# Kernel optimization log

Measured on AMD Instinct MI355X. Metric: run time of the kernel, lower is better.

## Reference

```python
import jax, jax.numpy as jnp
import numpy as np

DK = 64

def setup_inputs() -> dict:
    key = jax.random.key(0)
    kq, kk, kv = jax.random.split(key, 3)
    B, S, dk, dv = 16, 2048, 64, 64
    q = jax.random.normal(kq, (B, S, dk), dtype=jnp.float32)
    k = jax.random.normal(kk, (B, S, dk), dtype=jnp.float32)
    v = jax.random.normal(kv, (B, S, dv), dtype=jnp.float32)
    return {"q": q, "k": k, "v": v}

def reference(q, k, v):
    # scores: [B, Sq, Sk], scaled by 1/sqrt(dk)
    scale = 1.0 / jnp.sqrt(jnp.asarray(DK, dtype=q.dtype))
    scores = jnp.einsum('bqd,bkd->bqk', q, k) * scale
    attn = jax.nn.softmax(scores, axis=-1)
    return jnp.einsum('bqk,bkd->bqd', attn, v)
```

## Files before the change

kernel.cpp:

```cpp
#include <hip/hip_runtime.h>
#include <hip/hip_fp16.h>

#define SLEN 2048

typedef _Float16 half8_t  __attribute__((ext_vector_type(8)));
typedef __fp16   fp16x2_t __attribute__((ext_vector_type(2)));
typedef float    floatx16 __attribute__((ext_vector_type(16)));
typedef float    float2v  __attribute__((ext_vector_type(2)));

#define MFMA(a, b, c) __builtin_amdgcn_mfma_f32_32x32x16_f16((a), (b), (c), 0, 0, 0)

typedef const __attribute__((address_space(1))) void gvoid_t;
typedef __attribute__((address_space(3))) void lvoid_t;

__device__ __forceinline__ void gload_lds16(const void* g, void* l) {
    __builtin_amdgcn_global_load_lds((gvoid_t*)g, (lvoid_t*)l, 16, 0, 0);
}

__device__ __forceinline__ int bswap23(int r) {
    return (r & ~12) | ((r & 4) << 1) | ((r & 8) >> 1);
}

#define QSCALE 0.18033688011112042f
#define CINIT  -5.770780163555854f

__device__ __forceinline__ floatx16 zero16() {
    floatx16 z;
    #pragma unroll
    for (int i = 0; i < 16; ++i) z[i] = 0.0f;
    return z;
}

__device__ __forceinline__ floatx16 initC() {
    floatx16 z;
    #pragma unroll
    for (int i = 0; i < 16; ++i) z[i] = CINIT;
    return z;
}

union PU { fp16x2_t h2[4]; half8_t h8; };

__global__ __launch_bounds__(256)
void prep_kernel(const float* __restrict__ Kg, const float* __restrict__ Vg,
                 _Float16* __restrict__ KP, _Float16* __restrict__ VP)
{
    __shared__ _Float16 kt[32][72];
    __shared__ _Float16 vt[32][72];
    const int t = threadIdx.x;
    const int T = blockIdx.x;
    const size_t row0 = (size_t)T * 32;

    {
        const int r = t >> 3, c0 = (t & 7) * 8;
        const float* kp = Kg + (row0 + r) * 64 + c0;
        const float* vp = Vg + (row0 + r) * 64 + c0;
        float4 a0 = *(const float4*)kp;
        float4 a1 = *(const float4*)(kp + 4);
        float4 b0 = *(const float4*)vp;
        float4 b1 = *(const float4*)(vp + 4);
        kt[r][c0 + 0] = (_Float16)a0.x; kt[r][c0 + 1] = (_Float16)a0.y;
        kt[r][c0 + 2] = (_Float16)a0.z; kt[r][c0 + 3] = (_Float16)a0.w;
        kt[r][c0 + 4] = (_Float16)a1.x; kt[r][c0 + 5] = (_Float16)a1.y;
        kt[r][c0 + 6] = (_Float16)a1.z; kt[r][c0 + 7] = (_Float16)a1.w;
        vt[r][c0 + 0] = (_Float16)b0.x; vt[r][c0 + 1] = (_Float16)b0.y;
        vt[r][c0 + 2] = (_Float16)b0.z; vt[r][c0 + 3] = (_Float16)b0.w;
        vt[r][c0 + 4] = (_Float16)b1.x; vt[r][c0 + 5] = (_Float16)b1.y;
        vt[r][c0 + 6] = (_Float16)b1.z; vt[r][c0 + 7] = (_Float16)b1.w;
    }
    __syncthreads();

    const int hi  = (t >> 5) & 1;
    const int col = t & 31;

    {
        const int dc = t >> 6;
        half8_t ko;
        #pragma unroll
        for (int j = 0; j < 8; ++j) ko[j] = kt[col][dc * 16 + hi * 8 + j];
        *(half8_t*)(KP + (size_t)T * 2048 + t * 8) = ko;
    }
    {
        const int g = t >> 6, kc = g & 1, nc = g >> 1;
        half8_t vo;
        #pragma unroll
        for (int j = 0; j < 8; ++j)
            vo[j] = vt[bswap23(kc * 16 + hi * 8 + j)][nc * 32 + col];
        *(half8_t*)(VP + (size_t)T * 2048 + t * 8) = vo;
    }
}

__global__ __launch_bounds__(256, 2)
void fattn_kernel(const float* __restrict__ Qg, const _Float16* __restrict__ KP,
                  const _Float16* __restrict__ VP, float* __restrict__ Og)
{
    __shared__ __align__(16) _Float16 ring[4 * 2 * 4096];
    __shared__ float lbufl[4][2][32];
    __shared__ float lbuf2[2][32];

    const int tid  = threadIdx.x;
    const int w    = tid >> 6;
    const int lane = tid & 63;
    const int h    = lane >> 5;
    const int col  = lane & 31;

    const int p  = blockIdx.x;
    const int b  = ((p >> 8) << 3) | (p & 7);
    const int qb = (p >> 3) & 31;

    half8_t qh[2][4];
    #pragma unroll
    for (int s = 0; s < 2; ++s) {
        const size_t qrow = (size_t)b * SLEN + (size_t)qb * 64 + s * 32 + col;
        const float* qp = Qg + qrow * 64 + h * 8;
        #pragma unroll
        for (int dc = 0; dc < 4; ++dc) {
            float4 f0 = *(const float4*)(qp + dc * 16);
            float4 f1 = *(const float4*)(qp + dc * 16 + 4);
            float v[8] = {f0.x, f0.y, f0.z, f0.w, f1.x, f1.y, f1.z, f1.w};
            #pragma unroll
            for (int j = 0; j < 8; ++j)
                qh[s][dc][j] = (_Float16)(v[j] * QSCALE);
        }
    }

    _Float16* myring = ring + w * 8192;
    const char* KPb = (const char*)KP;
    const char* VPb = (const char*)VP;

    auto stage = [&](int buf, int t) {
        const size_t off = ((size_t)(b * 64 + w * 16 + t)) << 12;
        const char* ks = KPb + off + lane * 16;
        const char* vs = VPb + off + lane * 16;
        _Float16* d = myring + buf * 4096;
        gload_lds16(ks,        d);
        gload_lds16(ks + 1024, d + 512);
        gload_lds16(ks + 2048, d + 1024);
        gload_lds16(ks + 3072, d + 1536);
        gload_lds16(vs,        d + 2048);
        gload_lds16(vs + 1024, d + 2560);
        gload_lds16(vs + 2048, d + 3072);
        gload_lds16(vs + 3072, d + 3584);
    };

    floatx16 o00 = zero16(), o01 = zero16(), o10 = zero16(), o11 = zero16();
    float2v la0A = {0.0f, 0.0f}, la0B = {0.0f, 0.0f};
    float2v la1A = {0.0f, 0.0f}, la1B = {0.0f, 0.0f};

    stage(0, 0);

#define EXPPK(SS, U, J, ACC) {                                        \
    float e0 = __builtin_amdgcn_exp2f(SS[2*(J)]);                     \
    float e1 = __builtin_amdgcn_exp2f(SS[2*(J)+1]);                   \
    float2v e2 = {e0, e1};                                            \
    ACC += e2;                                                        \
    (U).h2[(J) & 3] = __builtin_amdgcn_cvt_pkrtz(e0, e1); }

    for (int t = 0; t < 16; ++t) {
        const int cur = t & 1;
        if (t < 15) {
            stage(1 - cur, t + 1);
            asm volatile("s_waitcnt vmcnt(8)" ::: "memory");
        } else {
            asm volatile("s_waitcnt vmcnt(0)" ::: "memory");
        }

        _Float16* kb = myring + cur * 4096;
        _Float16* vb = kb + 2048;

        half8_t kf[4];
        #pragma unroll
        for (int dc = 0; dc < 4; ++dc)
            kf[dc] = *(half8_t*)(kb + dc * 512 + lane * 8);

        floatx16 sa0 = zero16(), sb0 = initC();
        floatx16 sa1 = zero16(), sb1 = initC();

        sa0 = MFMA(kf[0], qh[0][0], sa0);
        sb0 = MFMA(kf[2], qh[0][2], sb0);
        sa0 = MFMA(kf[1], qh[0][1], sa0);
        sb0 = MFMA(kf[3], qh[0][3], sb0);

        half8_t vf[4];
        #pragma unroll
        for (int g = 0; g < 4; ++g)
            vf[g] = *(half8_t*)(vb + g * 512 + lane * 8);

        floatx16 ss0 = sa0 + sb0;
        PU u0, u1;
        sa1 = MFMA(kf[0], qh[1][0], sa1);
        EXPPK(ss0, u0, 0, la0A) EXPPK(ss0, u0, 1, la0B)
        sb1 = MFMA(kf[2], qh[1][2], sb1);
        EXPPK(ss0, u0, 2, la0A) EXPPK(ss0, u0, 3, la0B)
        sa1 = MFMA(kf[1], qh[1][1], sa1);
        EXPPK(ss0, u1, 4, la0A) EXPPK(ss0, u1, 5, la0B)
        sb1 = MFMA(kf[3], qh[1][3], sb1);
        EXPPK(ss0, u1, 6, la0A) EXPPK(ss0, u1, 7, la0B)

        half8_t pf00 = u0.h8, pf01 = u1.h8;

        floatx16 ss1 = sa1 + sb1;
        PU u2, u3;
        o00 = MFMA(pf00, vf[0], o00);
        EXPPK(ss1, u2, 0, la1A) EXPPK(ss1, u2, 1, la1B)
        o01 = MFMA(pf00, vf[2], o01);
        EXPPK(ss1, u2, 2, la1A) EXPPK(ss1, u2, 3, la1B)
        o00 = MFMA(pf01, vf[1], o00);
        EXPPK(ss1, u3, 4, la1A) EXPPK(ss1, u3, 5, la1B)
        o01 = MFMA(pf01, vf[3], o01);
        EXPPK(ss1, u3, 6, la1A) EXPPK(ss1, u3, 7, la1B)

        half8_t pf10 = u2.h8, pf11 = u3.h8;

        o10 = MFMA(pf10, vf[0], o10);
        o11 = MFMA(pf10, vf[2], o11);
        o10 = MFMA(pf11, vf[1], o10);
        o11 = MFMA(pf11, vf[3], o11);
    }
#undef EXPPK

    float la0 = la0A[0] + la0A[1] + la0B[0] + la0B[1];
    float la1 = la1A[0] + la1A[1] + la1B[0] + la1B[1];

    float lw0 = la0 + __shfl_xor(la0, 32, 64);
    float lw1 = la1 + __shfl_xor(la1, 32, 64);

    float* cb = (float*)ring;

#define ODUMP(d, g, acc) { _Pragma("unroll") \
    for (int r = 0; r < 16; ++r) (d)[(((g)*16 + r)*2 + h)*32 + col] = (acc)[r]; }
#define OADD(d, g, acc) { _Pragma("unroll") \
    for (int r = 0; r < 16; ++r) (acc)[r] += (d)[(((g)*16 + r)*2 + h)*32 + col]; }

    __syncthreads();
    if (w >= 2) {
        float* d = cb + (w - 2) * 4096;
        ODUMP(d, 0, o00) ODUMP(d, 1, o01) ODUMP(d, 2, o10) ODUMP(d, 3, o11)
        if (h == 0) { lbufl[w][0][col] = lw0; lbufl[w][1][col] = lw1; }
    }
    __syncthreads();
    if (w < 2) {
        float* d = cb + w * 4096;
        OADD(d, 0, o00) OADD(d, 1, o01) OADD(d, 2, o10) OADD(d, 3, o11)
        lw0 += lbufl[w + 2][0][col];
        lw1 += lbufl[w + 2][1][col];
    }
    __syncthreads();
    if (w == 1) {
        ODUMP(cb, 0, o00) ODUMP(cb, 1, o01) ODUMP(cb, 2, o10) ODUMP(cb, 3, o11)
        if (h == 0) { lbufl[1][0][col] = lw0; lbufl[1][1][col] = lw1; }
    }
    __syncthreads();
    if (w == 0) {
        OADD(cb, 0, o00) OADD(cb, 1, o01) OADD(cb, 2, o10) OADD(cb, 3, o11)
        lw0 += lbufl[1][0][col];
        lw1 += lbufl[1][1][col];
        if (h == 0) { lbuf2[0][col] = lw0; lbuf2[1][col] = lw1; }
    }
    __syncthreads();
    if (w == 0) {
        float* ob = cb + 8192;
        #pragma unroll
        for (int r = 0; r < 16; ++r) {
            const int qr = (r & 3) + 8 * (r >> 2) + 4 * h;
            const float li0 = 1.0f / lbuf2[0][qr];
            const float li1 = 1.0f / lbuf2[1][qr];
            ob[(0 * 32 + qr) * 64 +  0 + col] = o00[r] * li0;
            ob[(0 * 32 + qr) * 64 + 32 + col] = o01[r] * li0;
            ob[(1 * 32 + qr) * 64 +  0 + col] = o10[r] * li1;
            ob[(1 * 32 + qr) * 64 + 32 + col] = o11[r] * li1;
        }
    }
    __syncthreads();
    {
        const float* ob = cb + 8192;
        const int q = tid >> 2, ch = tid & 3;
        float4 x0 = *(const float4*)(ob + q * 64 + ch * 16);
        float4 x1 = *(const float4*)(ob + q * 64 + ch * 16 + 4);
        float4 x2 = *(const float4*)(ob + q * 64 + ch * 16 + 8);
        float4 x3 = *(const float4*)(ob + q * 64 + ch * 16 + 12);
        float* op = Og + ((size_t)b * SLEN + (size_t)qb * 64 + q) * 64 + ch * 16;
        *(float4*)(op)      = x0;
        *(float4*)(op + 4)  = x1;
        *(float4*)(op + 8)  = x2;
        *(float4*)(op + 12) = x3;
    }
#undef ODUMP
#undef OADD
}

extern "C" void kernel_launch(void* const* d_in, const int* in_sizes, int n_in,
                              void* d_out, int out_size, void* d_ws, size_t ws_size,
                              hipStream_t stream) {
    const float* q = (const float*)d_in[0];
    const float* k = (const float*)d_in[1];
    const float* v = (const float*)d_in[2];
    float* o = (float*)d_out;

    _Float16* KP = (_Float16*)d_ws;
    _Float16* VP = KP + (size_t)1024 * 2048;
    (void)ws_size; (void)in_sizes; (void)n_in; (void)out_size;

    prep_kernel<<<dim3(1024), dim3(256), 0, stream>>>(k, v, KP, VP);
    fattn_kernel<<<dim3(512), dim3(256), 0, stream>>>(q, KP, VP, o);
}
```

Baseline: 103.9 us.

## Merge two query tiles per 512-thread block and split K/V wait counts

```diff
diff --git a/kernel.cpp b/kernel.cpp
--- a/kernel.cpp
+++ b/kernel.cpp
@@ -89,28 +89,30 @@
     }
 }
 
-__global__ __launch_bounds__(256, 2)
+__global__ __launch_bounds__(512, 2)
 void fattn_kernel(const float* __restrict__ Qg, const _Float16* __restrict__ KP,
                   const _Float16* __restrict__ VP, float* __restrict__ Og)
 {
-    __shared__ __align__(16) _Float16 ring[4 * 2 * 4096];
-    __shared__ float lbufl[4][2][32];
-    __shared__ float lbuf2[2][32];
+    __shared__ __align__(16) _Float16 ring[8 * 8192];
+    __shared__ float lbufl[2][4][2][32];
+    __shared__ float lbuf2[2][2][32];
 
     const int tid  = threadIdx.x;
     const int w    = tid >> 6;
     const int lane = tid & 63;
     const int h    = lane >> 5;
     const int col  = lane & 31;
+    const int quarter = w & 3;
+    const int qh      = w >> 2;
 
     const int p  = blockIdx.x;
-    const int b  = ((p >> 8) << 3) | (p & 7);
-    const int qb = (p >> 3) & 31;
-
-    half8_t qh[2][4];
+    const int b  = (p & 7) | ((p >> 7) << 3);
+    const int qb = (p >> 3) & 15;
+
+    half8_t qh_[2][4];
     #pragma unroll
     for (int s = 0; s < 2; ++s) {
-        const size_t qrow = (size_t)b * SLEN + (size_t)qb * 64 + s * 32 + col;
+        const size_t qrow = (size_t)b * SLEN + (size_t)qb * 128 + qh * 64 + s * 32 + col;
         const float* qp = Qg + qrow * 64 + h * 8;
         #pragma unroll
         for (int dc = 0; dc < 4; ++dc) {
@@ -119,7 +121,7 @@
             float v[8] = {f0.x, f0.y, f0.z, f0.w, f1.x, f1.y, f1.z, f1.w};
             #pragma unroll
             for (int j = 0; j < 8; ++j)
-                qh[s][dc][j] = (_Float16)(v[j] * QSCALE);
+                qh_[s][dc][j] = (_Float16)(v[j] * QSCALE);
         }
     }
 
@@ -128,7 +130,7 @@
     const char* VPb = (const char*)VP;
 
     auto stage = [&](int buf, int t) {
-        const size_t off = ((size_t)(b * 64 + w * 16 + t)) << 12;
+        const size_t off = ((size_t)(b * 64 + quarter * 16 + t)) << 12;
         const char* ks = KPb + off + lane * 16;
         const char* vs = VPb + off + lane * 16;
         _Float16* d = myring + buf * 4096;
@@ -146,6 +148,8 @@
     float2v la0A = {0.0f, 0.0f}, la0B = {0.0f, 0.0f};
     float2v la1A = {0.0f, 0.0f}, la1B = {0.0f, 0.0f};
 
+    if (qh) __builtin_amdgcn_s_sleep(15);
+
     stage(0, 0);
 
 #define EXPPK(SS, U, J, ACC) {                                        \
@@ -159,9 +163,9 @@
         const int cur = t & 1;
         if (t < 15) {
             stage(1 - cur, t + 1);
-            asm volatile("s_waitcnt vmcnt(8)" ::: "memory");
+            asm volatile("s_waitcnt vmcnt(12)" ::: "memory");
         } else {
-            asm volatile("s_waitcnt vmcnt(0)" ::: "memory");
+            asm volatile("s_waitcnt vmcnt(4)" ::: "memory");
         }
 
         _Float16* kb = myring + cur * 4096;
@@ -175,11 +179,13 @@
         floatx16 sa0 = zero16(), sb0 = initC();
         floatx16 sa1 = zero16(), sb1 = initC();
 
-        sa0 = MFMA(kf[0], qh[0][0], sa0);
-        sb0 = MFMA(kf[2], qh[0][2], sb0);
-        sa0 = MFMA(kf[1], qh[0][1], sa0);
-        sb0 = MFMA(kf[3], qh[0][3], sb0);
-
+        sa0 = MFMA(kf[0], qh_[0][0], sa0);
+        sb0 = MFMA(kf[2], qh_[0][2], sb0);
+        sa0 = MFMA(kf[1], qh_[0][1], sa0);
+        sb0 = MFMA(kf[3], qh_[0][3], sb0);
+
+        if (t < 15) asm volatile("s_waitcnt vmcnt(8)" ::: "memory");
+        else        asm volatile("s_waitcnt vmcnt(0)" ::: "memory");
         half8_t vf[4];
         #pragma unroll
         for (int g = 0; g < 4; ++g)
@@ -187,13 +193,13 @@
 
         floatx16 ss0 = sa0 + sb0;
         PU u0, u1;
-        sa1 = MFMA(kf[0], qh[1][0], sa1);
+        sa1 = MFMA(kf[0], qh_[1][0], sa1);
         EXPPK(ss0, u0, 0, la0A) EXPPK(ss0, u0, 1, la0B)
-        sb1 = MFMA(kf[2], qh[1][2], sb1);
+        sb1 = MFMA(kf[2], qh_[1][2], sb1);
         EXPPK(ss0, u0, 2, la0A) EXPPK(ss0, u0, 3, la0B)
-        sa1 = MFMA(kf[1], qh[1][1], sa1);
+        sa1 = MFMA(kf[1], qh_[1][1], sa1);
         EXPPK(ss0, u1, 4, la0A) EXPPK(ss0, u1, 5, la0B)
-        sb1 = MFMA(kf[3], qh[1][3], sb1);
+        sb1 = MFMA(kf[3], qh_[1][3], sb1);
         EXPPK(ss0, u1, 6, la0A) EXPPK(ss0, u1, 7, la0B)
 
         half8_t pf00 = u0.h8, pf01 = u1.h8;
@@ -224,7 +230,8 @@
     float lw0 = la0 + __shfl_xor(la0, 32, 64);
     float lw1 = la1 + __shfl_xor(la1, 32, 64);
 
-    float* cb = (float*)ring;
+    float* ringf = (float*)ring;
+    float* cb = ringf + qh * 8192;
 
 #define ODUMP(d, g, acc) { _Pragma("unroll") \
     for (int r = 0; r < 16; ++r) (d)[(((g)*16 + r)*2 + h)*32 + col] = (acc)[r]; }
@@ -232,38 +239,39 @@
     for (int r = 0; r < 16; ++r) (acc)[r] += (d)[(((g)*16 + r)*2 + h)*32 + col]; }
 
     __syncthreads();
-    if (w >= 2) {
-        float* d = cb + (w - 2) * 4096;
+    if (quarter >= 2) {
+        float* d = cb + (quarter - 2) * 4096;
         ODUMP(d, 0, o00) ODUMP(d, 1, o01) ODUMP(d, 2, o10) ODUMP(d, 3, o11)
-        if (h == 0) { lbufl[w][0][col] = lw0; lbufl[w][1][col] = lw1; }
-    }
-    __syncthreads();
-    if (w < 2) {
-        float* d = cb + w * 4096;
+        if (h == 0) { lbufl[qh][quarter][0][col] = lw0;
+                      lbufl[qh][quarter][1][col] = lw1; }
+    }
+    __syncthreads();
+    if (quarter < 2) {
+        float* d = cb + quarter * 4096;
         OADD(d, 0, o00) OADD(d, 1, o01) OADD(d, 2, o10) OADD(d, 3, o11)
-        lw0 += lbufl[w + 2][0][col];
-        lw1 += lbufl[w + 2][1][col];
-    }
-    __syncthreads();
-    if (w == 1) {
+        lw0 += lbufl[qh][quarter + 2][0][col];
+        lw1 += lbufl[qh][quarter + 2][1][col];
+    }
+    __syncthreads();
+    if (quarter == 1) {
         ODUMP(cb, 0, o00) ODUMP(cb, 1, o01) ODUMP(cb, 2, o10) ODUMP(cb, 3, o11)
-        if (h == 0) { lbufl[1][0][col] = lw0; lbufl[1][1][col] = lw1; }
-    }
-    __syncthreads();
-    if (w == 0) {
+        if (h == 0) { lbufl[qh][1][0][col] = lw0; lbufl[qh][1][1][col] = lw1; }
+    }
+    __syncthreads();
+    if (quarter == 0) {
         OADD(cb, 0, o00) OADD(cb, 1, o01) OADD(cb, 2, o10) OADD(cb, 3, o11)
-        lw0 += lbufl[1][0][col];
-        lw1 += lbufl[1][1][col];
-        if (h == 0) { lbuf2[0][col] = lw0; lbuf2[1][col] = lw1; }
-    }
-    __syncthreads();
-    if (w == 0) {
-        float* ob = cb + 8192;
+        lw0 += lbufl[qh][1][0][col];
+        lw1 += lbufl[qh][1][1][col];
+        if (h == 0) { lbuf2[qh][0][col] = lw0; lbuf2[qh][1][col] = lw1; }
+    }
+    __syncthreads();
+    if (quarter == 0) {
+        float* ob = ringf + 16384 + qh * 4096;
         #pragma unroll
         for (int r = 0; r < 16; ++r) {
             const int qr = (r & 3) + 8 * (r >> 2) + 4 * h;
-            const float li0 = 1.0f / lbuf2[0][qr];
-            const float li1 = 1.0f / lbuf2[1][qr];
+            const float li0 = 1.0f / lbuf2[qh][0][qr];
+            const float li1 = 1.0f / lbuf2[qh][1][qr];
             ob[(0 * 32 + qr) * 64 +  0 + col] = o00[r] * li0;
             ob[(0 * 32 + qr) * 64 + 32 + col] = o01[r] * li0;
             ob[(1 * 32 + qr) * 64 +  0 + col] = o10[r] * li1;
@@ -272,13 +280,13 @@
     }
     __syncthreads();
     {
-        const float* ob = cb + 8192;
-        const int q = tid >> 2, ch = tid & 3;
-        float4 x0 = *(const float4*)(ob + q * 64 + ch * 16);
-        float4 x1 = *(const float4*)(ob + q * 64 + ch * 16 + 4);
-        float4 x2 = *(const float4*)(ob + q * 64 + ch * 16 + 8);
-        float4 x3 = *(const float4*)(ob + q * 64 + ch * 16 + 12);
-        float* op = Og + ((size_t)b * SLEN + (size_t)qb * 64 + q) * 64 + ch * 16;
+        const int row = tid >> 2, ch = tid & 3;
+        const float* ob = ringf + 16384 + (row >> 6) * 4096 + (row & 63) * 64 + ch * 16;
+        float4 x0 = *(const float4*)(ob);
+        float4 x1 = *(const float4*)(ob + 4);
+        float4 x2 = *(const float4*)(ob + 8);
+        float4 x3 = *(const float4*)(ob + 12);
+        float* op = Og + ((size_t)b * SLEN + (size_t)qb * 128 + row) * 64 + ch * 16;
         *(float4*)(op)      = x0;
         *(float4*)(op + 4)  = x1;
         *(float4*)(op + 8)  = x2;
@@ -301,5 +309,5 @@
     (void)ws_size; (void)in_sizes; (void)n_in; (void)out_size;
 
     prep_kernel<<<dim3(1024), dim3(256), 0, stream>>>(k, v, KP, VP);
-    fattn_kernel<<<dim3(512), dim3(256), 0, stream>>>(q, KP, VP, o);
-}
+    fattn_kernel<<<dim3(256), dim3(512), 0, stream>>>(q, KP, VP, o);
+}
```

Result: no change. 103.7 us (-0.2%).

## Software-pipeline QK scores one tile ahead to overlap exp with MFMA

Applied to the files above, without the earlier changes.

```diff
diff --git a/kernel.cpp b/kernel.cpp
--- a/kernel.cpp
+++ b/kernel.cpp
@@ -146,7 +146,8 @@
     float2v la0A = {0.0f, 0.0f}, la0B = {0.0f, 0.0f};
     float2v la1A = {0.0f, 0.0f}, la1B = {0.0f, 0.0f};
 
-    stage(0, 0);
+    floatx16 ssP0, ssP1;
+    half8_t vfA[4], vfB[4];
 
 #define EXPPK(SS, U, J, ACC) {                                        \
     float e0 = __builtin_amdgcn_exp2f(SS[2*(J)]);                     \
@@ -155,67 +156,101 @@
     ACC += e2;                                                        \
     (U).h2[(J) & 3] = __builtin_amdgcn_cvt_pkrtz(e0, e1); }
 
-    for (int t = 0; t < 16; ++t) {
-        const int cur = t & 1;
-        if (t < 15) {
-            stage(1 - cur, t + 1);
-            asm volatile("s_waitcnt vmcnt(8)" ::: "memory");
-        } else {
-            asm volatile("s_waitcnt vmcnt(0)" ::: "memory");
-        }
-
-        _Float16* kb = myring + cur * 4096;
-        _Float16* vb = kb + 2048;
-
+    stage(0, 0);
+    asm volatile("s_waitcnt vmcnt(0)" ::: "memory");
+    {
         half8_t kf[4];
         #pragma unroll
         for (int dc = 0; dc < 4; ++dc)
-            kf[dc] = *(half8_t*)(kb + dc * 512 + lane * 8);
-
+            kf[dc] = *(half8_t*)(myring + dc * 512 + lane * 8);
+        #pragma unroll
+        for (int g = 0; g < 4; ++g)
+            vfA[g] = *(half8_t*)(myring + 2048 + g * 512 + lane * 8);
+        stage(1, 1);
         floatx16 sa0 = zero16(), sb0 = initC();
         floatx16 sa1 = zero16(), sb1 = initC();
-
         sa0 = MFMA(kf[0], qh[0][0], sa0);
         sb0 = MFMA(kf[2], qh[0][2], sb0);
         sa0 = MFMA(kf[1], qh[0][1], sa0);
         sb0 = MFMA(kf[3], qh[0][3], sb0);
-
-        half8_t vf[4];
-        #pragma unroll
-        for (int g = 0; g < 4; ++g)
-            vf[g] = *(half8_t*)(vb + g * 512 + lane * 8);
-
-        floatx16 ss0 = sa0 + sb0;
-        PU u0, u1;
         sa1 = MFMA(kf[0], qh[1][0], sa1);
-        EXPPK(ss0, u0, 0, la0A) EXPPK(ss0, u0, 1, la0B)
         sb1 = MFMA(kf[2], qh[1][2], sb1);
-        EXPPK(ss0, u0, 2, la0A) EXPPK(ss0, u0, 3, la0B)
         sa1 = MFMA(kf[1], qh[1][1], sa1);
-        EXPPK(ss0, u1, 4, la0A) EXPPK(ss0, u1, 5, la0B)
         sb1 = MFMA(kf[3], qh[1][3], sb1);
-        EXPPK(ss0, u1, 6, la0A) EXPPK(ss0, u1, 7, la0B)
-
-        half8_t pf00 = u0.h8, pf01 = u1.h8;
-
-        floatx16 ss1 = sa1 + sb1;
-        PU u2, u3;
-        o00 = MFMA(pf00, vf[0], o00);
-        EXPPK(ss1, u2, 0, la1A) EXPPK(ss1, u2, 1, la1B)
-        o01 = MFMA(pf00, vf[2], o01);
-        EXPPK(ss1, u2, 2, la1A) EXPPK(ss1, u2, 3, la1B)
-        o00 = MFMA(pf01, vf[1], o00);
-        EXPPK(ss1, u3, 4, la1A) EXPPK(ss1, u3, 5, la1B)
-        o01 = MFMA(pf01, vf[3], o01);
-        EXPPK(ss1, u3, 6, la1A) EXPPK(ss1, u3, 7, la1B)
-
-        half8_t pf10 = u2.h8, pf11 = u3.h8;
-
-        o10 = MFMA(pf10, vf[0], o10);
-        o11 = MFMA(pf10, vf[2], o11);
-        o10 = MFMA(pf11, vf[1], o10);
-        o11 = MFMA(pf11, vf[3], o11);
-    }
+        ssP0 = sa0 + sb0;
+        ssP1 = sa1 + sb1;
+    }
+
+#define BODY(T, VC, VN)                                                       \
+{                                                                             \
+    asm volatile("s_waitcnt vmcnt(0)" ::: "memory");     \
+    _Float16* nb = myring + (((T) + 1) & 1) * 4096;                           \
+    half8_t kf[4];                                                            \
+    _Pragma("unroll")                                                         \
+    for (int dc = 0; dc < 4; ++dc)                                            \
+        kf[dc] = *(half8_t*)(nb + dc * 512 + lane * 8);                       \
+    _Pragma("unroll")                                                         \
+    for (int g = 0; g < 4; ++g)                                               \
+        VN[g] = *(half8_t*)(nb + 2048 + g * 512 + lane * 8);                  \
+    if ((T) + 2 < 16) stage((T) & 1, (T) + 2);   \
+    floatx16 sa0 = zero16(), sb0 = initC();                                   \
+    floatx16 sa1 = zero16(), sb1 = initC();                                   \
+    PU u0, u1, u2, u3;                                                        \
+    sa0 = MFMA(kf[0], qh[0][0], sa0); EXPPK(ssP0, u0, 0, la0A)                \
+    sb0 = MFMA(kf[2], qh[0][2], sb0); EXPPK(ssP0, u0, 1, la0B)                \
+    sa0 = MFMA(kf[1], qh[0][1], sa0); EXPPK(ssP0, u0, 2, la0A)                \
+    sb0 = MFMA(kf[3], qh[0][3], sb0); EXPPK(ssP0, u0, 3, la0B)                \
+    half8_t pf00 = u0.h8;                                                     \
+    o00 = MFMA(pf00, VC[0], o00);     EXPPK(ssP0, u1, 4, la0A)                \
+    sa1 = MFMA(kf[0], qh[1][0], sa1); EXPPK(ssP0, u1, 5, la0B)                \
+    o01 = MFMA(pf00, VC[2], o01);     EXPPK(ssP0, u1, 6, la0A)                \
+    sb1 = MFMA(kf[2], qh[1][2], sb1); EXPPK(ssP0, u1, 7, la0B)                \
+    half8_t pf01 = u1.h8;                                                     \
+    o00 = MFMA(pf01, VC[1], o00);     EXPPK(ssP1, u2, 0, la1A)                \
+    sa1 = MFMA(kf[1], qh[1][1], sa1); EXPPK(ssP1, u2, 1, la1B)                \
+    o01 = MFMA(pf01, VC[3], o01);     EXPPK(ssP1, u2, 2, la1A)                \
+    sb1 = MFMA(kf[3], qh[1][3], sb1); EXPPK(ssP1, u2, 3, la1B)                \
+    half8_t pf10 = u2.h8;                                                     \
+    o10 = MFMA(pf10, VC[0], o10);     EXPPK(ssP1, u3, 4, la1A)                \
+    o11 = MFMA(pf10, VC[2], o11);     EXPPK(ssP1, u3, 5, la1B)                \
+    EXPPK(ssP1, u3, 6, la1A)          EXPPK(ssP1, u3, 7, la1B)                \
+    half8_t pf11 = u3.h8;                                                     \
+    o10 = MFMA(pf11, VC[1], o10);                                             \
+    o11 = MFMA(pf11, VC[3], o11);                                             \
+    ssP0 = sa0 + sb0;                                                         \
+    ssP1 = sa1 + sb1;                                                         \
+}
+
+    for (int t = 0; t < 14; t += 2) {
+        BODY(t,     vfA, vfB);
+        BODY(t + 1, vfB, vfA);
+    }
+    BODY(14, vfA, vfB);
+
+    {
+        PU u0, u1, u2, u3;
+        EXPPK(ssP0, u0, 0, la0A) EXPPK(ssP0, u0, 1, la0B)
+        EXPPK(ssP0, u0, 2, la0A) EXPPK(ssP0, u0, 3, la0B)
+        half8_t pf00 = u0.h8;
+        o00 = MFMA(pf00, vfB[0], o00);
+        EXPPK(ssP0, u1, 4, la0A) EXPPK(ssP0, u1, 5, la0B)
+        o01 = MFMA(pf00, vfB[2], o01);
+        EXPPK(ssP0, u1, 6, la0A) EXPPK(ssP0, u1, 7, la0B)
+        half8_t pf01 = u1.h8;
+        o00 = MFMA(pf01, vfB[1], o00);
+        EXPPK(ssP1, u2, 0, la1A) EXPPK(ssP1, u2, 1, la1B)
+        o01 = MFMA(pf01, vfB[3], o01);
+        EXPPK(ssP1, u2, 2, la1A) EXPPK(ssP1, u2, 3, la1B)
+        half8_t pf10 = u2.h8;
+        o10 = MFMA(pf10, vfB[0], o10);
+        EXPPK(ssP1, u3, 4, la1A) EXPPK(ssP1, u3, 5, la1B)
+        o11 = MFMA(pf10, vfB[2], o11);
+        EXPPK(ssP1, u3, 6, la1A) EXPPK(ssP1, u3, 7, la1B)
+        half8_t pf11 = u3.h8;
+        o10 = MFMA(pf11, vfB[1], o10);
+        o11 = MFMA(pf11, vfB[3], o11);
+    }
+#undef BODY
 #undef EXPPK
 
     float la0 = la0A[0] + la0A[1] + la0B[0] + la0B[1];
```

After: 166.7 us. +60.4%, slower.
